# Performance work log

Hardware: AMD Instinct MI355X
Metric: run time of the kernel (lower is better)

## Reference

```python
import jax, jax.numpy as jnp
import numpy as np

B, K, U, I, D = 16384, 64, 100000, 100000, 256

def setup_inputs() -> dict:
    key = jax.random.key(0)
    k1, k2, k3, k4, k5, k6, k7, k8 = jax.random.split(key, 8)
    return {
        "nodes_u": jax.random.randint(k1, (B,), 0, U),
        "nodes_v": jax.random.randint(k2, (B,), 0, I),
        "neighbors": jax.random.randint(k3, (B, K), 0, U),
        "neighbor_counts": jax.random.randint(k4, (B,), 0, K + 1),
        "u2e": jax.random.normal(k5, (U, D), dtype=jnp.float32),
        "v2e": jax.random.normal(k6, (I, D), dtype=jnp.float32),
        "W": jax.random.normal(k7, (D, 2 * D), dtype=jnp.float32) * 0.05,  # torch Linear weight [out, in]
        "b": jax.random.normal(k8, (D,), dtype=jnp.float32) * 0.05,
    }

def reference(nodes_u, nodes_v, neighbors, neighbor_counts, u2e, v2e, W, b):
    # self embeddings [B, D]
    self_emb = u2e[nodes_u]
    # gather padded neighbor embeddings [B, K, D]
    neib_emb = u2e[neighbors]
    k_ = neighbors.shape[1]
    mask = jnp.arange(k_)[None, :] < neighbor_counts[:, None]          # [B, K] valid-neighbor mask
    nsum = jnp.einsum('bkd,bk->bd', neib_emb, mask.astype(neib_emb.dtype))
    cnt = jnp.maximum(neighbor_counts, 1).astype(self_emb.dtype)[:, None]
    nmean = nsum / cnt                                                  # mean-pool over valid neighbors
    cat = jnp.concatenate([self_emb, nmean], axis=1)                    # [B, 2D]
    proj = cat @ W.T + b                                                # Linear(2D -> D)
    # users with no neighbors use raw self embedding (matches `if len(neibs) > 0` branch)
    uemb = jnp.where((neighbor_counts > 0)[:, None], proj, self_emb)
    scores = jnp.sum(uemb * v2e[nodes_v], axis=1)                       # [B]
    return scores
```

## Files before the change

### kernel.cpp

```cpp
#include <hip/hip_runtime.h>

#define B_ROWS   16384
#define K_NB     64
#define D_DIM    256
#define TWO_D    512
#define R_BLK    8
#define THREADS  256

__global__ __launch_bounds__(THREADS)
void easyrec_fused(const int* __restrict__ nodes_u,
                   const int* __restrict__ nodes_v,
                   const int* __restrict__ neighbors,
                   const int* __restrict__ neighbor_counts,
                   const float* __restrict__ u2e,
                   const float* __restrict__ v2e,
                   const float* __restrict__ W,
                   const float* __restrict__ bias,
                   float* __restrict__ out)
{
    __shared__ int   nbr_lds[R_BLK * K_NB];
    __shared__ __align__(16) float cat_lds[R_BLK][TWO_D];
    __shared__ float red_lds[R_BLK * 4];
    __shared__ float selfdot_lds[R_BLK];
    __shared__ float bdot_lds[R_BLK];

    const int t    = threadIdx.x;
    const int wave = t >> 6;
    const int lane = t & 63;
    const int row0 = blockIdx.x * R_BLK;

    nbr_lds[t]           = neighbors[(size_t)row0 * K_NB + t];
    nbr_lds[t + THREADS] = neighbors[(size_t)row0 * K_NB + t + THREADS];
    __syncthreads();

    for (int rr = 0; rr < 2; ++rr) {
        const int r   = wave + rr * 4;
        const int row = row0 + r;
        const int nu  = __builtin_amdgcn_readfirstlane(nodes_u[row]);
        const int nv  = __builtin_amdgcn_readfirstlane(nodes_v[row]);
        const int cnt = __builtin_amdgcn_readfirstlane(neighbor_counts[row]);

        const float4 self4 = *(const float4*)(u2e + (size_t)nu * D_DIM + 4 * lane);
        const float4 v4    = *(const float4*)(v2e + (size_t)nv * D_DIM + 4 * lane);
        const float4 b4    = *(const float4*)(bias + 4 * lane);

        float4 acc = make_float4(0.f, 0.f, 0.f, 0.f);
        for (int k = 0; k < cnt; ++k) {
            const int idx = nbr_lds[r * K_NB + k];
            const float4 nb4 = *(const float4*)(u2e + (size_t)idx * D_DIM + 4 * lane);
            acc.x += nb4.x; acc.y += nb4.y; acc.z += nb4.z; acc.w += nb4.w;
        }
        const float inv = 1.0f / (float)(cnt > 0 ? cnt : 1);
        float4 nm = make_float4(acc.x * inv, acc.y * inv, acc.z * inv, acc.w * inv);

        *(float4*)(&cat_lds[r][4 * lane])         = self4;
        *(float4*)(&cat_lds[r][D_DIM + 4 * lane]) = nm;

        float sv = self4.x * v4.x + self4.y * v4.y + self4.z * v4.z + self4.w * v4.w;
        float bv = b4.x * v4.x + b4.y * v4.y + b4.z * v4.z + b4.w * v4.w;
        #pragma unroll
        for (int off = 32; off > 0; off >>= 1) {
            sv += __shfl_xor(sv, off, 64);
            bv += __shfl_xor(bv, off, 64);
        }
        if (lane == 0) { selfdot_lds[r] = sv; bdot_lds[r] = bv; }
    }
    __syncthreads();

    const float* vrow[R_BLK];
    #pragma unroll
    for (int r = 0; r < R_BLK; ++r) {
        const int nv = __builtin_amdgcn_readfirstlane(nodes_v[row0 + r]);
        vrow[r] = v2e + (size_t)nv * D_DIM;
    }

    float2 acc2[R_BLK];
    #pragma unroll
    for (int r = 0; r < R_BLK; ++r) acc2[r] = make_float2(0.f, 0.f);

    for (int d = 0; d < D_DIM; d += 4) {
        float4 vq[R_BLK];
        #pragma unroll
        for (int r = 0; r < R_BLK; ++r) vq[r] = *(const float4*)(vrow[r] + d);

        #pragma unroll
        for (int dd = 0; dd < 4; ++dd) {
            const float2 wq = *(const float2*)(W + (size_t)(d + dd) * TWO_D + 2 * t);
            #pragma unroll
            for (int r = 0; r < R_BLK; ++r) {
                const float vs = (dd == 0) ? vq[r].x : (dd == 1) ? vq[r].y
                               : (dd == 2) ? vq[r].z : vq[r].w;
                acc2[r].x += wq.x * vs;
                acc2[r].y += wq.y * vs;
            }
        }
    }

    #pragma unroll
    for (int r = 0; r < R_BLK; ++r) {
        const float2 c2 = *(const float2*)(&cat_lds[r][2 * t]);
        float p = c2.x * acc2[r].x + c2.y * acc2[r].y;
        #pragma unroll
        for (int off = 32; off > 0; off >>= 1) p += __shfl_xor(p, off, 64);
        if (lane == 0) red_lds[r * 4 + wave] = p;
    }
    __syncthreads();

    if (t < R_BLK) {
        const int row = row0 + t;
        const int cnt = neighbor_counts[row];
        float s;
        if (cnt > 0) {
            s = red_lds[t * 4 + 0] + red_lds[t * 4 + 1]
              + red_lds[t * 4 + 2] + red_lds[t * 4 + 3] + bdot_lds[t];
        } else {
            s = selfdot_lds[t];
        }
        out[row] = s;
    }
}

extern "C" void kernel_launch(void* const* d_in, const int* in_sizes, int n_in,
                              void* d_out, int out_size, void* d_ws, size_t ws_size,
                              hipStream_t stream) {
    const int*   nodes_u         = (const int*)d_in[0];
    const int*   nodes_v         = (const int*)d_in[1];
    const int*   neighbors       = (const int*)d_in[2];
    const int*   neighbor_counts = (const int*)d_in[3];
    const float* u2e             = (const float*)d_in[4];
    const float* v2e             = (const float*)d_in[5];
    const float* W               = (const float*)d_in[6];
    const float* bias            = (const float*)d_in[7];
    float*       out             = (float*)d_out;

    const int blocks = B_ROWS / R_BLK;
    easyrec_fused<<<blocks, THREADS, 0, stream>>>(
        nodes_u, nodes_v, neighbors, neighbor_counts, u2e, v2e, W, bias, out);
}
```

Measured before the change: 325.0 us.

## Double-buffer neighbor gathers through LDS with global_load_lds async copies

Replaces the serial per-neighbor gather loop with groups of four direct global-to-LDS loads per wave, double-buffered so the next group's loads are in flight while the current group is summed. The self/v dot products are hoisted before the gather for both rows. This aims to raise memory-level parallelism on the latency-bound random embedding gather. It adds 32 KB of LDS staging per block, which may reduce occupancy, and relies on manual vmcnt waits, with tail groups masked but still loaded from padded neighbor indices.

```diff
diff --git a/kernel.cpp b/kernel.cpp
--- a/kernel.cpp
+++ b/kernel.cpp
@@ -6,6 +6,15 @@
 #define TWO_D    512
 #define R_BLK    8
 #define THREADS  256
+#define NSLOT    8
+
+#define GLD16(g, l)                                                          \
+    __builtin_amdgcn_global_load_lds(                                        \
+        (const __attribute__((address_space(1))) void*)(g),                  \
+        (__attribute__((address_space(3))) void*)(l), 16, 0, 0)
+
+#define WAIT_VMCNT_0() asm volatile("s_waitcnt vmcnt(0)" ::: "memory")
+#define WAIT_VMCNT_4() asm volatile("s_waitcnt vmcnt(4)" ::: "memory")
 
 __global__ __launch_bounds__(THREADS)
 void easyrec_fused(const int* __restrict__ nodes_u,
@@ -18,8 +27,9 @@
                    const float* __restrict__ bias,
                    float* __restrict__ out)
 {
-    __shared__ int   nbr_lds[R_BLK * K_NB];
+    __shared__ __align__(16) int   nbr_lds[R_BLK * K_NB];
     __shared__ __align__(16) float cat_lds[R_BLK][TWO_D];
+    __shared__ __align__(16) float stage[4][NSLOT * D_DIM];
     __shared__ float red_lds[R_BLK * 4];
     __shared__ float selfdot_lds[R_BLK];
     __shared__ float bdot_lds[R_BLK];
@@ -28,42 +38,93 @@
     const int wave = t >> 6;
     const int lane = t & 63;
     const int row0 = blockIdx.x * R_BLK;
+    const int col  = 4 * lane;
+    float* const st = &stage[wave][0];
 
     nbr_lds[t]           = neighbors[(size_t)row0 * K_NB + t];
     nbr_lds[t + THREADS] = neighbors[(size_t)row0 * K_NB + t + THREADS];
     __syncthreads();
 
+    const int r0 = wave, r1 = wave + 4;
+    const int cnt0 = __builtin_amdgcn_readfirstlane(neighbor_counts[row0 + r0]);
+    const int cnt1 = __builtin_amdgcn_readfirstlane(neighbor_counts[row0 + r1]);
+    {
+        const float4 b4 = *(const float4*)(bias + col);
+        #pragma unroll
+        for (int rr = 0; rr < 2; ++rr) {
+            const int r  = (rr == 0) ? r0 : r1;
+            const int nu = __builtin_amdgcn_readfirstlane(nodes_u[row0 + r]);
+            const int nv = __builtin_amdgcn_readfirstlane(nodes_v[row0 + r]);
+            const float4 self4 = *(const float4*)(u2e + (size_t)nu * D_DIM + col);
+            const float4 v4    = *(const float4*)(v2e + (size_t)nv * D_DIM + col);
+            *(float4*)(&cat_lds[r][col]) = self4;
+            float sv = self4.x * v4.x + self4.y * v4.y + self4.z * v4.z + self4.w * v4.w;
+            float bv = b4.x * v4.x + b4.y * v4.y + b4.z * v4.z + b4.w * v4.w;
+            #pragma unroll
+            for (int off = 32; off > 0; off >>= 1) {
+                sv += __shfl_xor(sv, off, 64);
+                bv += __shfl_xor(bv, off, 64);
+            }
+            if (lane == 0) { selfdot_lds[r] = sv; bdot_lds[r] = bv; }
+        }
+    }
+
+    #pragma unroll
     for (int rr = 0; rr < 2; ++rr) {
-        const int r   = wave + rr * 4;
-        const int row = row0 + r;
-        const int nu  = __builtin_amdgcn_readfirstlane(nodes_u[row]);
-        const int nv  = __builtin_amdgcn_readfirstlane(nodes_v[row]);
-        const int cnt = __builtin_amdgcn_readfirstlane(neighbor_counts[row]);
-
-        const float4 self4 = *(const float4*)(u2e + (size_t)nu * D_DIM + 4 * lane);
-        const float4 v4    = *(const float4*)(v2e + (size_t)nv * D_DIM + 4 * lane);
-        const float4 b4    = *(const float4*)(bias + 4 * lane);
-
+        const int r   = (rr == 0) ? r0 : r1;
+        const int cnt = (rr == 0) ? cnt0 : cnt1;
         float4 acc = make_float4(0.f, 0.f, 0.f, 0.f);
-        for (int k = 0; k < cnt; ++k) {
-            const int idx = nbr_lds[r * K_NB + k];
-            const float4 nb4 = *(const float4*)(u2e + (size_t)idx * D_DIM + 4 * lane);
-            acc.x += nb4.x; acc.y += nb4.y; acc.z += nb4.z; acc.w += nb4.w;
+
+        if (cnt > 0) {
+            const int base = r * K_NB;
+            const int G = (cnt + 3) >> 2;
+
+            WAIT_VMCNT_0();
+
+            {
+                const int4 ia = *(const int4*)&nbr_lds[base];
+                GLD16(u2e + (size_t)ia.x * D_DIM + col, st + 0 * D_DIM);
+                GLD16(u2e + (size_t)ia.y * D_DIM + col, st + 1 * D_DIM);
+                GLD16(u2e + (size_t)ia.z * D_DIM + col, st + 2 * D_DIM);
+                GLD16(u2e + (size_t)ia.w * D_DIM + col, st + 3 * D_DIM);
+            }
+            for (int g = 0; g < G; ++g) {
+                const int cur = (g & 1) * 4;
+                if (g + 1 < G) {
+                    const int nxt = ((g + 1) & 1) * 4;
+                    const int4 ia = *(const int4*)&nbr_lds[base + 4 * (g + 1)];
+                    GLD16(u2e + (size_t)ia.x * D_DIM + col, st + (nxt + 0) * D_DIM);
+                    GLD16(u2e + (size_t)ia.y * D_DIM + col, st + (nxt + 1) * D_DIM);
+                    GLD16(u2e + (size_t)ia.z * D_DIM + col, st + (nxt + 2) * D_DIM);
+                    GLD16(u2e + (size_t)ia.w * D_DIM + col, st + (nxt + 3) * D_DIM);
+                    WAIT_VMCNT_4();
+                } else {
+                    WAIT_VMCNT_0();
+                }
+                const float4 n0 = *(const float4*)(st + (cur + 0) * D_DIM + col);
+                const float4 n1 = *(const float4*)(st + (cur + 1) * D_DIM + col);
+                const float4 n2 = *(const float4*)(st + (cur + 2) * D_DIM + col);
+                const float4 n3 = *(const float4*)(st + (cur + 3) * D_DIM + col);
+                if (4 * g + 4 <= cnt) {
+                    acc.x += n0.x + n1.x + n2.x + n3.x;
+                    acc.y += n0.y + n1.y + n2.y + n3.y;
+                    acc.z += n0.z + n1.z + n2.z + n3.z;
+                    acc.w += n0.w + n1.w + n2.w + n3.w;
+                } else {
+                    const float m0 = (4 * g + 0 < cnt) ? 1.f : 0.f;
+                    const float m1 = (4 * g + 1 < cnt) ? 1.f : 0.f;
+                    const float m2 = (4 * g + 2 < cnt) ? 1.f : 0.f;
+                    const float m3 = (4 * g + 3 < cnt) ? 1.f : 0.f;
+                    acc.x += n0.x * m0 + n1.x * m1 + n2.x * m2 + n3.x * m3;
+                    acc.y += n0.y * m0 + n1.y * m1 + n2.y * m2 + n3.y * m3;
+                    acc.z += n0.z * m0 + n1.z * m1 + n2.z * m2 + n3.z * m3;
+                    acc.w += n0.w * m0 + n1.w * m1 + n2.w * m2 + n3.w * m3;
+                }
+            }
         }
         const float inv = 1.0f / (float)(cnt > 0 ? cnt : 1);
-        float4 nm = make_float4(acc.x * inv, acc.y * inv, acc.z * inv, acc.w * inv);
-
-        *(float4*)(&cat_lds[r][4 * lane])         = self4;
-        *(float4*)(&cat_lds[r][D_DIM + 4 * lane]) = nm;
-
-        float sv = self4.x * v4.x + self4.y * v4.y + self4.z * v4.z + self4.w * v4.w;
-        float bv = b4.x * v4.x + b4.y * v4.y + b4.z * v4.z + b4.w * v4.w;
-        #pragma unroll
-        for (int off = 32; off > 0; off >>= 1) {
-            sv += __shfl_xor(sv, off, 64);
-            bv += __shfl_xor(bv, off, 64);
-        }
-        if (lane == 0) { selfdot_lds[r] = sv; bdot_lds[r] = bv; }
+        *(float4*)(&cat_lds[r][D_DIM + col]) =
+            make_float4(acc.x * inv, acc.y * inv, acc.z * inv, acc.w * inv);
     }
     __syncthreads();
 
```

Measured after the change: 341.8 us. 5.2% more time.
